# Performance work log

Measured on AMD Instinct MI355X. Metric: run time of the kernel, lower is better.

## Reference

```python
import jax, jax.numpy as jnp
import numpy as np

B, C, H, W = 8, 256, 64, 64
CR = C // 8  # reduced channels = 32


def setup_inputs() -> dict:
    key = jax.random.key(0)
    k1, k2, k3, k4 = jax.random.split(key, 4)
    x = jax.random.normal(k1, (B, C, H, W), dtype=jnp.float32)
    # 1x1 conv weights (bias=False) are plain channel matmuls; scale like kaiming (~1/sqrt(fan_in))
    Wt = jax.random.normal(k2, (3 * CR, C), dtype=jnp.float32) * (1.0 / np.sqrt(C))
    Wo = jax.random.normal(k3, (C, CR), dtype=jnp.float32) * (1.0 / np.sqrt(CR))
    scale = jax.random.normal(k4, (1,), dtype=jnp.float32)
    return {"x": x, "Wt": Wt, "Wo": Wo, "scale": scale}


def reference(x, Wt, Wo, scale):
    b, c, h, w = x.shape
    n = h * w
    # 1x1 conv QKV projection: [B, 3*Cr, H, W]
    t = jnp.einsum('oc,bchw->bohw', Wt, x)
    cr = t.shape[1] // 3
    key = t[:, :cr].reshape(b, cr, n)          # [B, Cr, N]
    query = t[:, cr:2 * cr].reshape(b, cr, n)  # [B, Cr, N]
    value = t[:, 2 * cr:].reshape(b, cr, n)    # [B, Cr, N]
    # scores[b, i, j] = sum_c key[b,c,i] * query[b,c,j]  (key^T @ query)
    scores = jnp.einsum('bci,bcj->bij', key, query)  # [B, N, N]
    # torch Softmax(dim=1): normalize over the key axis i
    weights = jax.nn.softmax(scores, axis=1)
    # output[b, c, j] = sum_i value[b,c,i] * weights[b,i,j]
    out = jnp.einsum('bci,bij->bcj', value, weights)  # [B, Cr, N]
    out = out.reshape(b, cr, h, w)
    out = jnp.einsum('oc,bchw->bohw', Wo, out)  # 1x1 conv back to C channels
    return scale[0] * out + x
```

## Files before the change

kernel.cpp:

```cpp
#include <hip/hip_runtime.h>
#include <math.h>

#define B_ 8
#define C_ 256
#define CR_ 32
#define N_ 4096
#define NH_ 4

typedef __attribute__((ext_vector_type(8))) short bf16x8;
typedef __attribute__((ext_vector_type(4))) short bf16x4;
typedef __attribute__((ext_vector_type(4))) float f32x4;
typedef __attribute__((ext_vector_type(16))) float f32x16;
typedef __attribute__((ext_vector_type(2))) unsigned uint32x2;

#if defined(__has_builtin)
#if __has_builtin(__builtin_amdgcn_permlane32_swap)
#define HAVE_PLSWAP 1
#endif
#endif

__device__ inline short f2bf(float f) {
  union { float f; unsigned u; } v; v.f = f;
  unsigned r = v.u + 0x7FFFu + ((v.u >> 16) & 1u);
  return (short)(r >> 16);
}
__device__ inline float bf2f(short h) {
  union { unsigned u; float f; } v; v.u = ((unsigned)(unsigned short)h) << 16;
  return v.f;
}
__device__ inline short f2bf_r(float f) {
  return (short)((__float_as_uint(f) + 0x8000u) >> 16);
}


__global__ __launch_bounds__(256) void prep_weights(const float* __restrict__ Wt,
                                                    const float* __restrict__ Wo,
                                                    const float* __restrict__ scale,
                                                    short* __restrict__ WtHi,
                                                    short* __restrict__ WtLo,
                                                    short* __restrict__ WoB) {
  const int blk = blockIdx.x, tid = threadIdx.x;
  if (blk < 96) {
    float v = Wt[blk * C_ + tid];
    if (blk >= 32 && blk < 64) v *= 1.44269504f;
    const short h = f2bf(v);
    WtHi[blk * C_ + tid] = h;
    WtLo[blk * C_ + tid] = f2bf(v - bf2f(h));
  } else {
    const int idx = (blk - 96) * 256 + tid;
    WoB[idx] = f2bf(Wo[idx] * scale[0]);
  }
}

__global__ __launch_bounds__(256) void qkv_mfma(const float* __restrict__ x,
                                                const short* __restrict__ WtHi,
                                                const short* __restrict__ WtLo,
                                                short* __restrict__ Kf,
                                                short* __restrict__ Qf,
                                                short* __restrict__ Vf) {
  const int b = blockIdx.y;
  const int tid = threadIdx.x;
  const int wave = tid >> 6, lane = tid & 63;
  const int col = lane & 15, quad = lane >> 4;
  const int n0 = (blockIdx.x * 4 + wave) * 16;

  const f32x4 z4 = {0.f, 0.f, 0.f, 0.f};
  f32x4 acc[6] = {z4, z4, z4, z4, z4, z4};

  const float* xb = x + (size_t)b * C_ * N_ + n0 + col;
  float xcur[8], xnxt[8];
#pragma unroll
  for (int j = 0; j < 8; ++j) xcur[j] = xb[(size_t)(quad * 8 + j) * N_];

#pragma unroll 2
  for (int c0 = 0; c0 < C_; c0 += 32) {
    if (c0 < C_ - 32) {
#pragma unroll
      for (int j = 0; j < 8; ++j)
        xnxt[j] = xb[(size_t)(c0 + 32 + quad * 8 + j) * N_];
    }
    bf16x8 xh, xl;
#pragma unroll
    for (int j = 0; j < 8; ++j) {
      const short h = (short)(__float_as_uint(xcur[j]) >> 16);
      xh[j] = h;
      xl[j] = f2bf_r(xcur[j] - bf2f(h));
    }
#pragma unroll
    for (int ot = 0; ot < 4; ++ot) {
      const int off = (ot * 16 + col) * C_ + c0 + quad * 8;
      const bf16x8 bh = *(const bf16x8*)(WtHi + off);
      const bf16x8 bl = *(const bf16x8*)(WtLo + off);
      acc[ot] = __builtin_amdgcn_mfma_f32_16x16x32_bf16(xh, bh, acc[ot], 0, 0, 0);
      acc[ot] = __builtin_amdgcn_mfma_f32_16x16x32_bf16(xl, bh, acc[ot], 0, 0, 0);
      acc[ot] = __builtin_amdgcn_mfma_f32_16x16x32_bf16(xh, bl, acc[ot], 0, 0, 0);
    }
#pragma unroll
    for (int ct = 0; ct < 2; ++ct) {
      const int off = ((64 + ct * 16) + col) * C_ + c0 + quad * 8;
      const bf16x8 ah = *(const bf16x8*)(WtHi + off);
      const bf16x8 al = *(const bf16x8*)(WtLo + off);
      acc[4 + ct] = __builtin_amdgcn_mfma_f32_16x16x32_bf16(ah, xh, acc[4 + ct], 0, 0, 0);
      acc[4 + ct] = __builtin_amdgcn_mfma_f32_16x16x32_bf16(ah, xl, acc[4 + ct], 0, 0, 0);
      acc[4 + ct] = __builtin_amdgcn_mfma_f32_16x16x32_bf16(al, xh, acc[4 + ct], 0, 0, 0);
    }
#pragma unroll
    for (int j = 0; j < 8; ++j) xcur[j] = xnxt[j];
  }

#pragma unroll
  for (int ot = 0; ot < 2; ++ot)
#pragma unroll
    for (int r = 0; r < 4; ++r) {
      const int i = n0 + quad * 4 + r;
      const int c = ot * 16 + col;
      const int ln = (i & 31) | (((c >> 3) & 1) << 5);
      Kf[(((size_t)(b * 128 + (i >> 5)) * 2 + (c >> 4)) * 64 + ln) * 8 + (c & 7)] =
          f2bf(acc[ot][r]);
    }
#pragma unroll
  for (int ot = 2; ot < 4; ++ot)
#pragma unroll
    for (int r = 0; r < 4; ++r) {
      const int j = n0 + quad * 4 + r;
      const int c = (ot - 2) * 16 + col;
      const int ln = (j & 31) | (((c >> 3) & 1) << 5);
      Qf[(((size_t)(b * 128 + (j >> 5)) * 2 + (c >> 4)) * 64 + ln) * 8 + (c & 7)] =
          f2bf(acc[ot][r]);
    }
#pragma unroll
  for (int ct = 0; ct < 2; ++ct)
#pragma unroll
    for (int r = 0; r < 4; ++r) {
      const int c = ct * 16 + quad * 4 + r;
      const int n = n0 + col;
      const int ln = c | (((n >> 3) & 1) << 5);
      Vf[((size_t)(b * 256 + (n >> 4)) * 64 + ln) * 8 + (n & 7)] =
          f2bf(acc[4 + ct][r]);
    }
}

__global__ __launch_bounds__(64, 4) void flash_attn(const short* __restrict__ Kf,
                                                    const short* __restrict__ Qf,
                                                    const short* __restrict__ Vf,
                                                    short* __restrict__ OPart,
                                                    float* __restrict__ LPart) {
  const int b = blockIdx.z, hq = blockIdx.y;
  const int jt = blockIdx.x;
  const int lane = threadIdx.x;
  const int j32 = lane & 31, h32 = lane >> 5;

  const f32x16 z16 = {0.f};
  const short* pQ = Qf + ((size_t)(b * 128 + jt) * 2) * 512 + lane * 8;
  const bf16x8 qf0 = *(const bf16x8*)(pQ);
  const bf16x8 qf1 = *(const bf16x8*)(pQ + 512);

  const short* pK = Kf + ((size_t)(b * 128 + hq * 32) * 2) * 512 + lane * 8;
  const short* pV = Vf + ((size_t)(b * 256 + hq * 64)) * 512 + lane * 8;

  f32x16 acc = z16;
  float ps = 0.f;

  bf16x8 ka = *(const bf16x8*)(pK);
  bf16x8 kb = *(const bf16x8*)(pK + 512);
  bf16x8 va = *(const bf16x8*)(pV);
  bf16x8 vb = *(const bf16x8*)(pV + 512);

#pragma unroll 1
  for (int t = 0; t < 32; ++t) {
    pK += 1024;
    pV += 1024;
    const bf16x8 kan = *(const bf16x8*)(pK);
    const bf16x8 kbn = *(const bf16x8*)(pK + 512);
    const bf16x8 van = *(const bf16x8*)(pV);
    const bf16x8 vbn = *(const bf16x8*)(pV + 512);

    __builtin_amdgcn_s_setprio(1);
    f32x16 s = __builtin_amdgcn_mfma_f32_32x32x16_bf16(ka, qf0, z16, 0, 0, 0);
    s = __builtin_amdgcn_mfma_f32_32x32x16_bf16(kb, qf1, s, 0, 0, 0);
    __builtin_amdgcn_s_setprio(0);
    float p[16];
#pragma unroll
    for (int r = 0; r < 16; ++r) p[r] = __builtin_amdgcn_exp2f(s[r]);
    ps += (((p[0] + p[1]) + (p[2] + p[3])) + ((p[4] + p[5]) + (p[6] + p[7]))) +
          (((p[8] + p[9]) + (p[10] + p[11])) + ((p[12] + p[13]) + (p[14] + p[15])));
    unsigned d[8];
#pragma unroll
    for (int k = 0; k < 8; ++k) {
      const unsigned u0 = __float_as_uint(p[2 * k]) + 0x8000u;
      const unsigned u1 = __float_as_uint(p[2 * k + 1]) + 0x8000u;
      d[k] = __builtin_amdgcn_perm(u1, u0, 0x07060302u);
    }
    union { unsigned u[4]; bf16x8 v; } f0, f1;
#ifdef HAVE_PLSWAP
    {
      const uint32x2 r0 = __builtin_amdgcn_permlane32_swap(d[0], d[2], false, false);
      f0.u[0] = r0[0]; f0.u[2] = r0[1];
      const uint32x2 r1 = __builtin_amdgcn_permlane32_swap(d[1], d[3], false, false);
      f0.u[1] = r1[0]; f0.u[3] = r1[1];
      const uint32x2 r2 = __builtin_amdgcn_permlane32_swap(d[4], d[6], false, false);
      f1.u[0] = r2[0]; f1.u[2] = r2[1];
      const uint32x2 r3 = __builtin_amdgcn_permlane32_swap(d[5], d[7], false, false);
      f1.u[1] = r3[0]; f1.u[3] = r3[1];
    }
#else
    {
      unsigned xw[8];
#pragma unroll
      for (int k = 0; k < 8; ++k) xw[k] = __shfl_xor((int)d[k], 32);
      f0.u[0] = h32 ? xw[2] : d[0];
      f0.u[1] = h32 ? xw[3] : d[1];
      f0.u[2] = h32 ? d[2] : xw[0];
      f0.u[3] = h32 ? d[3] : xw[1];
      f1.u[0] = h32 ? xw[6] : d[4];
      f1.u[1] = h32 ? xw[7] : d[5];
      f1.u[2] = h32 ? d[6] : xw[4];
      f1.u[3] = h32 ? d[7] : xw[5];
    }
#endif
    __builtin_amdgcn_s_setprio(1);
    acc = __builtin_amdgcn_mfma_f32_32x32x16_bf16(va, f0.v, acc, 0, 0, 0);
    acc = __builtin_amdgcn_mfma_f32_32x32x16_bf16(vb, f1.v, acc, 0, 0, 0);
    __builtin_amdgcn_s_setprio(0);

    ka = kan; kb = kbn; va = van; vb = vbn;
  }

  const size_t base = ((size_t)b * NH_ + hq) * N_;
  const float l = ps + __shfl_xor(ps, 32);
  const int jg = jt * 32 + j32;
  if (h32 == 0) LPart[base + jg] = l;
  short* OP = OPart + (base + jg) * 32;
#pragma unroll
  for (int g = 0; g < 4; ++g) {
    bf16x4 o = {f2bf(acc[4 * g + 0]), f2bf(acc[4 * g + 1]),
                f2bf(acc[4 * g + 2]), f2bf(acc[4 * g + 3])};
    *(bf16x4*)(OP + 8 * g + 4 * h32) = o;
  }
}

__global__ __launch_bounds__(256) void out_proj(const short* __restrict__ OPart,
                                                const float* __restrict__ LPart,
                                                const short* __restrict__ WoB,
                                                const float* __restrict__ x,
                                                float* __restrict__ out) {
  const int b = blockIdx.z, chalf = blockIdx.y;
  const int tid = threadIdx.x;
  const int wave = tid >> 6, lane = tid & 63;
  const int col = lane & 15, quad = lane >> 4;
  const int jg = blockIdx.x * 64 + wave * 16 + col;
  const int n0 = blockIdx.x * 64 + wave * 16;

  float osum[8];
#pragma unroll
  for (int e = 0; e < 8; ++e) osum[e] = 0.f;
  float lsum = 0.f;
#pragma unroll
  for (int h = 0; h < NH_; ++h) {
    const size_t p = ((size_t)b * NH_ + h) * N_ + jg;
    const bf16x8 o = *(const bf16x8*)(OPart + p * 32 + quad * 8);
#pragma unroll
    for (int e = 0; e < 8; ++e) osum[e] += bf2f(o[e]);
    lsum += LPart[p];
  }
  const float linv = 1.f / lsum;
  bf16x8 bf;
#pragma unroll
  for (int e = 0; e < 8; ++e) bf[e] = f2bf(osum[e] * linv);

  const f32x4 z4 = {0.f, 0.f, 0.f, 0.f};
  const float* xb = x + (size_t)b * C_ * N_;
  float* ob = out + (size_t)b * C_ * N_;
#pragma unroll
  for (int ct = 0; ct < 8; ++ct) {
    const int ctg = chalf * 8 + ct;
    const bf16x8 af = *(const bf16x8*)(WoB + (ctg * 16 + col) * 32 + quad * 8);
    const f32x4 a = __builtin_amdgcn_mfma_f32_16x16x32_bf16(af, bf, z4, 0, 0, 0);
#pragma unroll
    for (int r = 0; r < 4; ++r) {
      const size_t idx = (size_t)(ctg * 16 + quad * 4 + r) * N_ + n0 + col;
      ob[idx] = a[r] + xb[idx];
    }
  }
}

extern "C" void kernel_launch(void* const* d_in, const int* in_sizes, int n_in,
                              void* d_out, int out_size, void* d_ws,
                              size_t ws_size, hipStream_t stream) {
  const float* x = (const float*)d_in[0];
  const float* Wt = (const float*)d_in[1];
  const float* Wo = (const float*)d_in[2];
  const float* scale = (const float*)d_in[3];
  float* out = (float*)d_out;

  short* OPart = (short*)d_ws;
  float* LPart = (float*)(OPart + (size_t)B_ * NH_ * N_ * 32);
  short* Kf = (short*)(LPart + (size_t)B_ * NH_ * N_);
  short* Qf = Kf + (size_t)B_ * 128 * 1024;
  short* Vf = Qf + (size_t)B_ * 128 * 1024;
  short* WtHi = Vf + (size_t)B_ * 256 * 512;
  short* WtLo = WtHi + 96 * C_;
  short* WoB = WtLo + 96 * C_;

  prep_weights<<<dim3(128), 256, 0, stream>>>(Wt, Wo, scale, WtHi, WtLo, WoB);
  qkv_mfma<<<dim3(64, B_), 256, 0, stream>>>(x, WtHi, WtLo, Kf, Qf, Vf);
  flash_attn<<<dim3(128, NH_, B_), 64, 0, stream>>>(Kf, Qf, Vf, OPart, LPart);
  out_proj<<<dim3(64, 2, B_), 256, 0, stream>>>(OPart, LPart, WoB, x, out);
}
```

Before: 152.3 us.

## Split attention keys into eight partitions, pair waves per block, use packed bf16 convert

Doubles the number of key-axis partitions (NH 4→8) so each wave walks 16 key tiles instead of 32, giving twice as many independent waves to fill the GPU. Blocks now hold two 64-lane waves covering adjacent query tiles. V loads move into the loop body instead of being prefetched one iteration ahead. The manual round-and-perm bf16 packing is replaced with the v_cvt_pk_bf16_f32 instruction. Partial outputs and sums double in size, which adds work and traffic in the out_proj reduction.

```diff
diff --git a/kernel.cpp b/kernel.cpp
--- a/kernel.cpp
+++ b/kernel.cpp
@@ -5,7 +5,7 @@
 #define C_ 256
 #define CR_ 32
 #define N_ 4096
-#define NH_ 4
+#define NH_ 8
 
 typedef __attribute__((ext_vector_type(8))) short bf16x8;
 typedef __attribute__((ext_vector_type(4))) short bf16x4;
@@ -30,6 +30,12 @@
 }
 __device__ inline short f2bf_r(float f) {
   return (short)((__float_as_uint(f) + 0x8000u) >> 16);
+}
+
+__device__ inline unsigned cvt_pk_bf16(float a, float b) {
+  unsigned d;
+  asm("v_cvt_pk_bf16_f32 %0, %1, %2" : "=v"(d) : "v"(a), "v"(b));
+  return d;
 }
 
 
@@ -140,14 +146,15 @@
     }
 }
 
-__global__ __launch_bounds__(64, 4) void flash_attn(const short* __restrict__ Kf,
-                                                    const short* __restrict__ Qf,
-                                                    const short* __restrict__ Vf,
-                                                    short* __restrict__ OPart,
-                                                    float* __restrict__ LPart) {
+__global__ __launch_bounds__(128) void flash_attn(const short* __restrict__ Kf,
+                                                  const short* __restrict__ Qf,
+                                                  const short* __restrict__ Vf,
+                                                  short* __restrict__ OPart,
+                                                  float* __restrict__ LPart) {
   const int b = blockIdx.z, hq = blockIdx.y;
-  const int jt = blockIdx.x;
-  const int lane = threadIdx.x;
+  const int tid = threadIdx.x;
+  const int jt = blockIdx.x * 2 + (tid >> 6);
+  const int lane = tid & 63;
   const int j32 = lane & 31, h32 = lane >> 5;
 
   const f32x16 z16 = {0.f};
@@ -155,25 +162,23 @@
   const bf16x8 qf0 = *(const bf16x8*)(pQ);
   const bf16x8 qf1 = *(const bf16x8*)(pQ + 512);
 
-  const short* pK = Kf + ((size_t)(b * 128 + hq * 32) * 2) * 512 + lane * 8;
-  const short* pV = Vf + ((size_t)(b * 256 + hq * 64)) * 512 + lane * 8;
+  const short* pK = Kf + ((size_t)(b * 128 + hq * 16) * 2) * 512 + lane * 8;
+  const short* pV = Vf + ((size_t)(b * 256 + hq * 32)) * 512 + lane * 8;
 
   f32x16 acc = z16;
   float ps = 0.f;
 
   bf16x8 ka = *(const bf16x8*)(pK);
   bf16x8 kb = *(const bf16x8*)(pK + 512);
-  bf16x8 va = *(const bf16x8*)(pV);
-  bf16x8 vb = *(const bf16x8*)(pV + 512);
 
 #pragma unroll 1
-  for (int t = 0; t < 32; ++t) {
+  for (int t = 0; t < 16; ++t) {
+    const bf16x8 va = *(const bf16x8*)(pV);
+    const bf16x8 vb = *(const bf16x8*)(pV + 512);
     pK += 1024;
     pV += 1024;
     const bf16x8 kan = *(const bf16x8*)(pK);
     const bf16x8 kbn = *(const bf16x8*)(pK + 512);
-    const bf16x8 van = *(const bf16x8*)(pV);
-    const bf16x8 vbn = *(const bf16x8*)(pV + 512);
 
     __builtin_amdgcn_s_setprio(1);
     f32x16 s = __builtin_amdgcn_mfma_f32_32x32x16_bf16(ka, qf0, z16, 0, 0, 0);
@@ -184,28 +189,31 @@
     for (int r = 0; r < 16; ++r) p[r] = __builtin_amdgcn_exp2f(s[r]);
     ps += (((p[0] + p[1]) + (p[2] + p[3])) + ((p[4] + p[5]) + (p[6] + p[7]))) +
           (((p[8] + p[9]) + (p[10] + p[11])) + ((p[12] + p[13]) + (p[14] + p[15])));
-    unsigned d[8];
-#pragma unroll
-    for (int k = 0; k < 8; ++k) {
-      const unsigned u0 = __float_as_uint(p[2 * k]) + 0x8000u;
-      const unsigned u1 = __float_as_uint(p[2 * k + 1]) + 0x8000u;
-      d[k] = __builtin_amdgcn_perm(u1, u0, 0x07060302u);
-    }
     union { unsigned u[4]; bf16x8 v; } f0, f1;
 #ifdef HAVE_PLSWAP
     {
-      const uint32x2 r0 = __builtin_amdgcn_permlane32_swap(d[0], d[2], false, false);
+      const unsigned d0 = cvt_pk_bf16(p[0], p[1]);
+      const unsigned d1 = cvt_pk_bf16(p[2], p[3]);
+      const unsigned d2 = cvt_pk_bf16(p[4], p[5]);
+      const unsigned d3 = cvt_pk_bf16(p[6], p[7]);
+      const uint32x2 r0 = __builtin_amdgcn_permlane32_swap(d0, d2, false, false);
       f0.u[0] = r0[0]; f0.u[2] = r0[1];
-      const uint32x2 r1 = __builtin_amdgcn_permlane32_swap(d[1], d[3], false, false);
+      const uint32x2 r1 = __builtin_amdgcn_permlane32_swap(d1, d3, false, false);
       f0.u[1] = r1[0]; f0.u[3] = r1[1];
-      const uint32x2 r2 = __builtin_amdgcn_permlane32_swap(d[4], d[6], false, false);
+      const unsigned d4 = cvt_pk_bf16(p[8], p[9]);
+      const unsigned d5 = cvt_pk_bf16(p[10], p[11]);
+      const unsigned d6 = cvt_pk_bf16(p[12], p[13]);
+      const unsigned d7 = cvt_pk_bf16(p[14], p[15]);
+      const uint32x2 r2 = __builtin_amdgcn_permlane32_swap(d4, d6, false, false);
       f1.u[0] = r2[0]; f1.u[2] = r2[1];
-      const uint32x2 r3 = __builtin_amdgcn_permlane32_swap(d[5], d[7], false, false);
+      const uint32x2 r3 = __builtin_amdgcn_permlane32_swap(d5, d7, false, false);
       f1.u[1] = r3[0]; f1.u[3] = r3[1];
     }
 #else
     {
-      unsigned xw[8];
+      unsigned d[8], xw[8];
+#pragma unroll
+      for (int k = 0; k < 8; ++k) d[k] = cvt_pk_bf16(p[2 * k], p[2 * k + 1]);
 #pragma unroll
       for (int k = 0; k < 8; ++k) xw[k] = __shfl_xor((int)d[k], 32);
       f0.u[0] = h32 ? xw[2] : d[0];
@@ -223,7 +231,8 @@
     acc = __builtin_amdgcn_mfma_f32_32x32x16_bf16(vb, f1.v, acc, 0, 0, 0);
     __builtin_amdgcn_s_setprio(0);
 
-    ka = kan; kb = kbn; va = van; vb = vbn;
+    ka = kan;
+    kb = kbn;
   }
 
   const size_t base = ((size_t)b * NH_ + hq) * N_;
@@ -304,6 +313,6 @@
 
   prep_weights<<<dim3(128), 256, 0, stream>>>(Wt, Wo, scale, WtHi, WtLo, WoB);
   qkv_mfma<<<dim3(64, B_), 256, 0, stream>>>(x, WtHi, WtLo, Kf, Qf, Vf);
-  flash_attn<<<dim3(128, NH_, B_), 64, 0, stream>>>(Kf, Qf, Vf, OPart, LPart);
+  flash_attn<<<dim3(64, NH_, B_), 128, 0, stream>>>(Kf, Qf, Vf, OPart, LPart);
   out_proj<<<dim3(64, 2, B_), 256, 0, stream>>>(OPart, LPart, WoB, x, out);
 }
```

After: 156.2 us. +2.6%, slower.
